# Kernel tuning notes

Measured on AMD Instinct MI355X. Metric: run time of the kernel, lower is better.

## Reference

```python
import jax, jax.numpy as jnp
import numpy as np

H = 16  # num_heads


def setup_inputs() -> dict:
    key = jax.random.key(0)
    ks = jax.random.split(key, 12)
    B, S, D = 2, 2048, 1024
    init = lambda k, shape: (jax.random.normal(k, shape, dtype=jnp.float32) * 0.02)
    return {
        "x": jax.random.normal(ks[0], (B, S, D), dtype=jnp.float32),
        "wq": init(ks[1], (D, D)), "bq": init(ks[2], (D,)),
        "wk": init(ks[3], (D, D)), "bk": init(ks[4], (D,)),
        "wv": init(ks[5], (D, D)), "bv": init(ks[6], (D,)),
        "wo": init(ks[7], (D, D)), "bo": init(ks[8], (D,)),
        "w3d": init(ks[9], (3, D)), "b3d": init(ks[10], (3,)),
    }


def _pairwise_l2(pos):
    # pos: [B,S,3] -> [B,S,S] Euclidean distance (safe sqrt: zero grad at 0, like torch.cdist)
    sq = jnp.sum((pos[:, :, None, :] - pos[:, None, :, :]) ** 2, axis=-1)
    safe = jnp.where(sq > 0, sq, 1.0)
    return jnp.where(sq > 0, jnp.sqrt(safe), 0.0)


def reference(x, wq, bq, wk, bk, wv, bv, wo, bo, w3d, b3d):
    B, S, D = x.shape
    hd = D // H
    scale = 1.0 / (hd ** 0.5)
    # V projection -> [B,H,S,hd]  (Q/K are computed in torch forward but unused in APPROX scores)
    V = (x @ wv.T + bv).reshape(B, S, H, hd).transpose(0, 2, 1, 3)
    # 3D semantic positions and non-dot-product scores (identical across heads)
    pos = x @ w3d.T + b3d                      # [B,S,3]
    dist = _pairwise_l2(pos)                   # [B,S,S]
    scores = -dist[:, None, :, :] * scale      # [B,H,S,S] (broadcast over heads)
    causal = jnp.triu(jnp.ones((S, S), dtype=bool), k=1)
    scores = jnp.where(causal[None, None], -jnp.inf, scores)
    attn = jax.nn.softmax(scores, axis=-1)
    attn = jnp.nan_to_num(attn, nan=0.0)
    out = jnp.einsum('bhqk,bhkd->bhqd', attn, V)  # [B,H,S,hd]
    out = out.transpose(0, 2, 1, 3).reshape(B, S, D)
    return out @ wo.T + bo
```

## Files before the change

### kernel.cpp

```cpp
#include <hip/hip_runtime.h>
#include <hip/hip_bf16.h>
#include <stdint.h>


typedef __attribute__((ext_vector_type(8))) short bf16x8;
typedef __attribute__((ext_vector_type(4))) float f32x4;
typedef __attribute__((ext_vector_type(4))) unsigned short us4;

#define AS1(p) (const __attribute__((address_space(1))) unsigned int*)(p)
#define AS3(p) (__attribute__((address_space(3))) unsigned int*)(p)

__device__ __forceinline__ unsigned short f2bf(float f) {
  union { float f; unsigned u; } v; v.f = f;
  unsigned r = v.u + 0x7FFFu + ((v.u >> 16) & 1u);
  return (unsigned short)(r >> 16);
}

__global__ void k_prep(const float* __restrict__ x, const float* __restrict__ wv,
                       const float* __restrict__ wo, const float* __restrict__ bv,
                       const float* __restrict__ bo, const float* __restrict__ w3d,
                       const float* __restrict__ b3d,
                       unsigned short* __restrict__ xT, unsigned short* __restrict__ wvT,
                       unsigned short* __restrict__ wob, float* __restrict__ cvec,
                       float* __restrict__ pos) {
  __shared__ __align__(16) float lsm[64 * 68];
  const int bx = blockIdx.x, t = threadIdx.x;
  if (bx < 1024) {
    const int b = bx >> 9, rest = bx & 511, st = rest >> 4, dt = rest & 15;
    const int s0 = st * 64, d0 = dt * 64;
    const int r = t >> 2, c4 = t & 3;
    const float* src = x + (size_t)(b * 2048 + s0 + r) * 1024 + d0;
    float (*ld)[68] = (float(*)[68])lsm;
    #pragma unroll
    for (int p = 0; p < 4; p++)
      *(float4*)&ld[r][(c4 + 4 * p) * 4] = ((const float4*)src)[c4 + 4 * p];
    __syncthreads();
    #pragma unroll
    for (int p = 0; p < 4; p++) {
      const int dl = (t >> 4) + (p << 4);
      us4 o;
      #pragma unroll
      for (int k = 0; k < 4; k++)
        ((unsigned short*)&o)[k] = f2bf(ld[(t & 15) * 4 + k][dl]);
      *(us4*)(xT + ((size_t)b << 21) + (size_t)(d0 + dl) * 2048 + s0 + (t & 15) * 4) = o;
    }
  } else if (bx < 2048) {
    const int bb = bx - 1024, tr = bb >> 5, tc = bb & 31;
    const int r = t >> 5, c = t & 31;
    float (*ld)[33] = (float(*)[33])lsm;
    #pragma unroll
    for (int rr = r; rr < 32; rr += 8)
      ld[rr][c] = wv[(size_t)(tr * 32 + rr) * 1024 + tc * 32 + c];
    __syncthreads();
    #pragma unroll
    for (int rr = r; rr < 32; rr += 8)
      wvT[(size_t)(tc * 32 + rr) * 1024 + tr * 32 + c] = f2bf(ld[c][rr]);
  } else if (bx < 3072) {
    const int oo = bx - 2048;
    const float4 w = ((const float4*)(wo + (size_t)oo * 1024))[t];
    us4 ob; ob.x = f2bf(w.x); ob.y = f2bf(w.y); ob.z = f2bf(w.z); ob.w = f2bf(w.w);
    ((us4*)(wob + (size_t)oo * 1024))[t] = ob;
    const float4 b = ((const float4*)bv)[t];
    float a = w.x * b.x + w.y * b.y + w.z * b.z + w.w * b.w;
    #pragma unroll
    for (int off = 32; off; off >>= 1) a += __shfl_down(a, off, 64);
    if ((t & 63) == 0) lsm[t >> 6] = a;
    __syncthreads();
    if (t == 0) cvec[oo] = lsm[0] + lsm[1] + lsm[2] + lsm[3] + bo[oo];
  } else {
    const int row = bx - 3072;
    const float4 xv = ((const float4*)(x + (size_t)row * 1024))[t];
    const float4 w0 = ((const float4*)(w3d))[t];
    const float4 w1 = ((const float4*)(w3d + 1024))[t];
    const float4 w2 = ((const float4*)(w3d + 2048))[t];
    float a0 = xv.x*w0.x + xv.y*w0.y + xv.z*w0.z + xv.w*w0.w;
    float a1 = xv.x*w1.x + xv.y*w1.y + xv.z*w1.z + xv.w*w1.w;
    float a2 = xv.x*w2.x + xv.y*w2.y + xv.z*w2.z + xv.w*w2.w;
    #pragma unroll
    for (int off = 32; off; off >>= 1) {
      a0 += __shfl_down(a0, off, 64);
      a1 += __shfl_down(a1, off, 64);
      a2 += __shfl_down(a2, off, 64);
    }
    if ((t & 63) == 0) { lsm[(t >> 6) * 3] = a0; lsm[(t >> 6) * 3 + 1] = a1; lsm[(t >> 6) * 3 + 2] = a2; }
    __syncthreads();
    if (t == 0) {
      pos[(size_t)row*3 + 0] = lsm[0] + lsm[3] + lsm[6] + lsm[9]  + b3d[0];
      pos[(size_t)row*3 + 1] = lsm[1] + lsm[4] + lsm[7] + lsm[10] + b3d[1];
      pos[(size_t)row*3 + 2] = lsm[2] + lsm[5] + lsm[8] + lsm[11] + b3d[2];
    }
  }
}

__global__ void k_attn(const float* __restrict__ pos, unsigned short* __restrict__ Ab) {
  const int row = blockIdx.x;
  const int q = row & 2047, bb = row >> 11;
  const float* pb = pos + ((size_t)bb << 11) * 3;
  const float qx = pb[q*3], qy = pb[q*3+1], qz = pb[q*3+2];
  const float4* pb4 = (const float4*)pb;
  const int jmax = ((q >> 7) + 1) << 7;
  float v[2][4];
  float sum = 0.f;
  #pragma unroll
  for (int cc = 0; cc < 2; cc++) {
    const int j0 = (cc << 10) + (threadIdx.x << 2);
    float e0 = 0.f, e1 = 0.f, e2 = 0.f, e3 = 0.f;
    if (j0 < jmax) {
      const float4 A4 = pb4[3*(j0 >> 2)], B4 = pb4[3*(j0 >> 2) + 1], C4 = pb4[3*(j0 >> 2) + 2];
      const float px[4] = {A4.x, A4.w, B4.z, C4.y};
      const float py[4] = {A4.y, B4.x, B4.w, C4.z};
      const float pz[4] = {A4.z, B4.y, C4.x, C4.w};
      float ee[4];
      #pragma unroll
      for (int u = 0; u < 4; u++) {
        float e = 0.f;
        if (j0 + u <= q) {
          float dx = qx - px[u], dy = qy - py[u], dz = qz - pz[u];
          float sq = fmaf(dx, dx, fmaf(dy, dy, dz*dz));
          float d = sq > 0.f ? sqrtf(sq) : 0.f;
          e = __expf(-0.125f * d);
        }
        ee[u] = e;
      }
      e0 = ee[0]; e1 = ee[1]; e2 = ee[2]; e3 = ee[3];
    }
    v[cc][0] = e0; v[cc][1] = e1; v[cc][2] = e2; v[cc][3] = e3;
    sum += e0 + e1 + e2 + e3;
  }
  #pragma unroll
  for (int off = 32; off; off >>= 1) sum += __shfl_down(sum, off, 64);
  __shared__ float red[4];
  if ((threadIdx.x & 63) == 0) red[threadIdx.x >> 6] = sum;
  __syncthreads();
  const float inv = 1.f / (red[0] + red[1] + red[2] + red[3]);
  unsigned short* orow = Ab + (size_t)row * 2048;
  #pragma unroll
  for (int cc = 0; cc < 2; cc++) {
    const int j0 = (cc << 10) + (threadIdx.x << 2);
    if (j0 < jmax) {
      us4 o;
      o.x = f2bf(v[cc][0]*inv); o.y = f2bf(v[cc][1]*inv);
      o.z = f2bf(v[cc][2]*inv); o.w = f2bf(v[cc][3]*inv);
      *(us4*)(orow + j0) = o;
    }
  }
}

template<int BM, int BN, int WM, int WN>
__device__ __forceinline__ void gemm_db(
    const unsigned short* __restrict__ A, int lda,
    const unsigned short* __restrict__ Bt, int ldb,
    int m0, int n0, int kmax,
    unsigned short* lds, f32x4* acc) {
  constexpr int WAVES = WM * WN;
  constexpr int FI = BM / (WM * 16), FJ = BN / (WN * 16);
  constexpr int CPW = ((BM + BN) / 8) / WAVES;
  constexpr int BUFSZ = (BM + BN) * 64;
  const int tid = threadIdx.x, l = tid & 63, w = tid >> 6;
  const int wm = w & (WM - 1), wn = w / WM;
  const int gcol = ((l & 7) ^ (l >> 3)) << 3;

  auto stage = [&](int buf, int k0) {
    unsigned short* base = lds + buf * BUFSZ;
    #pragma unroll
    for (int e = 0; e < CPW; ++e) {
      const int c = w * CPW + e;
      const unsigned short* src;
      unsigned short* dst;
      if (c < BM / 8) {
        src = A + (size_t)(m0 + c*8 + (l >> 3)) * lda + k0 + gcol;
        dst = base + c * 512;
      } else {
        const int cb = c - BM / 8;
        src = Bt + (size_t)(n0 + cb*8 + (l >> 3)) * ldb + k0 + gcol;
        dst = base + BM * 64 + cb * 512;
      }
      __builtin_amdgcn_global_load_lds(AS1(src), AS3(dst), 16, 0, 0);
    }
  };

  auto compute = [&](int buf) {
    unsigned short* lA = lds + buf * BUFSZ;
    unsigned short* lB = lA + BM * 64;
    #pragma unroll
    for (int h = 0; h < 2; ++h) {
      const int slot = ((h << 2) | (l >> 4)) ^ (l & 7);
      bf16x8 af[FI], bfr[FJ];
      #pragma unroll
      for (int i = 0; i < FI; ++i) {
        const int ar = wm * (BM / WM) + i * 16 + (l & 15);
        af[i] = *(const bf16x8*)&lA[ar * 64 + slot * 8];
      }
      #pragma unroll
      for (int j = 0; j < FJ; ++j) {
        const int br = wn * (BN / WN) + j * 16 + (l & 15);
        bfr[j] = *(const bf16x8*)&lB[br * 64 + slot * 8];
      }
      #pragma unroll
      for (int i = 0; i < FI; ++i)
        #pragma unroll
        for (int j = 0; j < FJ; ++j)
          acc[i * FJ + j] = __builtin_amdgcn_mfma_f32_16x16x32_bf16(af[i], bfr[j], acc[i * FJ + j], 0, 0, 0);
    }
  };

  const int NT = kmax >> 6;
  stage(0, 0);
  int cur = 0;
  for (int t = 0; t < NT; ++t) {
    if (t + 1 < NT) {
      stage(cur ^ 1, (t + 1) << 6);
      static_assert(CPW == 4 || CPW == 6 || CPW == 8, "vmcnt literal");
      if constexpr (CPW == 4) asm volatile("s_waitcnt vmcnt(4) lgkmcnt(0)" ::: "memory");
      else if constexpr (CPW == 6) asm volatile("s_waitcnt vmcnt(6) lgkmcnt(0)" ::: "memory");
      else asm volatile("s_waitcnt vmcnt(8) lgkmcnt(0)" ::: "memory");
    } else {
      asm volatile("s_waitcnt vmcnt(0) lgkmcnt(0)" ::: "memory");
    }
    __builtin_amdgcn_s_barrier();
    compute(cur);
    __builtin_amdgcn_s_barrier();
    cur ^= 1;
  }
}

__global__ __launch_bounds__(256, 3) void k_gemm_axwc(
    const unsigned short* __restrict__ Ab, const unsigned short* __restrict__ xT,
    unsigned short* __restrict__ Axb,
    const unsigned short* __restrict__ wob, const unsigned short* __restrict__ wvT,
    unsigned short* __restrict__ Wcs) {
  __shared__ __align__(16) unsigned short lds[2 * (128 + 64) * 64];
  const int bx = blockIdx.x;
  const int l = threadIdx.x & 63, w = threadIdx.x >> 6;
  const int wm = w & 1, wn = w >> 1;
  if (bx < 512) {
    f32x4 acc[8] = {};
    const int xcd = bx & 7, rest = bx >> 3;
    const int g = rest >> 4, n0i = rest & 15;
    const int mi = (g < 2) ? (15 - xcd) : xcd;
    const int b = g & 1;
    const int m0 = mi << 7, n0 = n0i << 6;
    const unsigned short* A  = Ab + ((size_t)b << 22);
    const unsigned short* Bt = xT + ((size_t)b << 21);
    gemm_db<128, 64, 2, 2>(A, 2048, Bt, 2048, m0, n0, (mi + 1) << 7, lds, acc);
    unsigned short* Obase = Axb + ((size_t)b << 11) * 1024;
    #pragma unroll
    for (int i = 0; i < 4; i++) {
      const int r0 = m0 + wm*64 + i*16 + ((l >> 4) << 2);
      #pragma unroll
      for (int j = 0; j < 2; j++) {
        const int cidx = n0 + wn*32 + j*16 + (l & 15);
        #pragma unroll
        for (int t = 0; t < 4; t++)
          Obase[(size_t)(r0 + t) * 1024 + cidx] = f2bf(acc[i*2 + j][t]);
      }
    }
  } else {
    f32x4 acc[4] = {};
    const int g = bx - 512;
    const int m0 = (g & 15) * 64, n0 = (g >> 4) * 64;
    gemm_db<64, 64, 2, 2>(wob, 1024, wvT, 1024, m0, n0, 1024, lds, acc);
    #pragma unroll
    for (int i = 0; i < 2; i++) {
      const int r0 = m0 + wm*32 + i*16 + ((l >> 4) << 2);
      #pragma unroll
      for (int j = 0; j < 2; j++) {
        const int cidx = n0 + wn*32 + j*16 + (l & 15);
        #pragma unroll
        for (int t = 0; t < 4; t++)
          Wcs[(size_t)(r0 + t) * 1024 + cidx] = f2bf(acc[i*2 + j][t]);
      }
    }
  }
}

__global__ __launch_bounds__(256, 2) void k_gemm_out(
    const unsigned short* __restrict__ Axb, const unsigned short* __restrict__ Wcs,
    const float* __restrict__ cvec, float* __restrict__ out) {
  __shared__ __align__(16) unsigned short lds[2 * (128 + 128) * 64];
  f32x4 acc[16] = {};
  const int m0 = blockIdx.x * 128, n0 = blockIdx.y * 128;
  gemm_db<128, 128, 2, 2>(Axb, 1024, Wcs, 1024, m0, n0, 1024, lds, acc);
  const int l = threadIdx.x & 63, w = threadIdx.x >> 6;
  const int wm = w & 1, wn = w >> 1;
  #pragma unroll
  for (int i = 0; i < 4; i++) {
    const int r0 = m0 + wm*64 + i*16 + ((l >> 4) << 2);
    #pragma unroll
    for (int j = 0; j < 4; j++) {
      const int cidx = n0 + wn*64 + j*16 + (l & 15);
      const float cv = cvec[cidx];
      #pragma unroll
      for (int t = 0; t < 4; t++)
        out[(size_t)(r0 + t) * 1024 + cidx] = acc[i*4 + j][t] + cv;
    }
  }
}

extern "C" void kernel_launch(void* const* d_in, const int* in_sizes, int n_in,
                              void* d_out, int out_size, void* d_ws, size_t ws_size,
                              hipStream_t stream) {
  const float* x   = (const float*)d_in[0];
  const float* wv  = (const float*)d_in[5];
  const float* bv  = (const float*)d_in[6];
  const float* wo  = (const float*)d_in[7];
  const float* bo  = (const float*)d_in[8];
  const float* w3d = (const float*)d_in[9];
  const float* b3d = (const float*)d_in[10];
  float* out = (float*)d_out;

  char* ws = (char*)d_ws;
  unsigned short* xT  = (unsigned short*)(ws);
  unsigned short* wvT = (unsigned short*)(ws + ( 8u << 20));
  unsigned short* wob = (unsigned short*)(ws + (10u << 20));
  unsigned short* Wcs = (unsigned short*)(ws + (12u << 20));
  unsigned short* Axb = (unsigned short*)(ws + (14u << 20));
  unsigned short* Ab  = (unsigned short*)(ws + (22u << 20));
  float*          pos = (float*)(ws + (38u << 20));
  float*          cvec= (float*)(ws + (39u << 20));

  k_prep<<<7168, 256, 0, stream>>>(x, wv, wo, bv, bo, w3d, b3d, xT, wvT, wob, cvec, pos);
  k_attn<<<4096, 256, 0, stream>>>(pos, Ab);
  k_gemm_axwc<<<768, 256, 0, stream>>>(Ab, xT, Axb, wob, wvT, Wcs);
  k_gemm_out<<<dim3(32, 8), 256, 0, stream>>>(Axb, Wcs, cvec, out);
}
```

Before: 57.67 us.

## Replace double-buffered GEMM loop with three-stage LDS ring in axwc kernel

Adds a gemm_ring variant that keeps two K-tiles of global-to-LDS loads in flight, using three LDS buffers, and issues each prefetch right after the barrier. This removes the second barrier per iteration. The goal is to hide more global load latency behind MFMA work. In exchange LDS per block grows by half and launch bounds drop from 3 to 2 blocks per CU, so occupancy may fall.

```diff
diff --git a/kernel.cpp b/kernel.cpp
--- a/kernel.cpp
+++ b/kernel.cpp
@@ -147,6 +147,85 @@
 }
 
 template<int BM, int BN, int WM, int WN>
+__device__ __forceinline__ void gemm_ring(
+    const unsigned short* __restrict__ A, int lda,
+    const unsigned short* __restrict__ Bt, int ldb,
+    int m0, int n0, int kmax,
+    unsigned short* lds, f32x4* acc) {
+  constexpr int WAVES = WM * WN;
+  constexpr int FI = BM / (WM * 16), FJ = BN / (WN * 16);
+  constexpr int CPW = ((BM + BN) / 8) / WAVES;
+  constexpr int BUFSZ = (BM + BN) * 64;
+  const int tid = threadIdx.x, l = tid & 63, w = tid >> 6;
+  const int wm = w & (WM - 1), wn = w / WM;
+  const int gcol = ((l & 7) ^ (l >> 3)) << 3;
+
+  auto stage = [&](int buf, int k0) {
+    unsigned short* base = lds + buf * BUFSZ;
+    #pragma unroll
+    for (int e = 0; e < CPW; ++e) {
+      const int c = w * CPW + e;
+      const unsigned short* src;
+      unsigned short* dst;
+      if (c < BM / 8) {
+        src = A + (size_t)(m0 + c*8 + (l >> 3)) * lda + k0 + gcol;
+        dst = base + c * 512;
+      } else {
+        const int cb = c - BM / 8;
+        src = Bt + (size_t)(n0 + cb*8 + (l >> 3)) * ldb + k0 + gcol;
+        dst = base + BM * 64 + cb * 512;
+      }
+      __builtin_amdgcn_global_load_lds(AS1(src), AS3(dst), 16, 0, 0);
+    }
+  };
+
+  auto compute = [&](int buf) {
+    unsigned short* lA = lds + buf * BUFSZ;
+    unsigned short* lB = lA + BM * 64;
+    #pragma unroll
+    for (int h = 0; h < 2; ++h) {
+      const int slot = ((h << 2) | (l >> 4)) ^ (l & 7);
+      bf16x8 af[FI], bfr[FJ];
+      #pragma unroll
+      for (int i = 0; i < FI; ++i) {
+        const int ar = wm * (BM / WM) + i * 16 + (l & 15);
+        af[i] = *(const bf16x8*)&lA[ar * 64 + slot * 8];
+      }
+      #pragma unroll
+      for (int j = 0; j < FJ; ++j) {
+        const int br = wn * (BN / WN) + j * 16 + (l & 15);
+        bfr[j] = *(const bf16x8*)&lB[br * 64 + slot * 8];
+      }
+      #pragma unroll
+      for (int i = 0; i < FI; ++i)
+        #pragma unroll
+        for (int j = 0; j < FJ; ++j)
+          acc[i * FJ + j] = __builtin_amdgcn_mfma_f32_16x16x32_bf16(af[i], bfr[j], acc[i * FJ + j], 0, 0, 0);
+    }
+  };
+
+  const int NT = kmax >> 6;
+  stage(0, 0);
+  if (NT > 1) stage(1, 64);
+  int cur = 0, nxt2 = 2;
+  for (int t = 0; t < NT; ++t) {
+    if (t < NT - 1) {
+      static_assert(CPW == 4 || CPW == 6 || CPW == 8, "vmcnt literal");
+      if constexpr (CPW == 4) asm volatile("s_waitcnt vmcnt(4) lgkmcnt(0)" ::: "memory");
+      else if constexpr (CPW == 6) asm volatile("s_waitcnt vmcnt(6) lgkmcnt(0)" ::: "memory");
+      else asm volatile("s_waitcnt vmcnt(8) lgkmcnt(0)" ::: "memory");
+    } else {
+      asm volatile("s_waitcnt vmcnt(0) lgkmcnt(0)" ::: "memory");
+    }
+    __builtin_amdgcn_s_barrier();
+    if (t + 2 < NT) stage(nxt2, (t + 2) << 6);
+    compute(cur);
+    cur = cur == 2 ? 0 : cur + 1;
+    nxt2 = nxt2 == 2 ? 0 : nxt2 + 1;
+  }
+}
+
+template<int BM, int BN, int WM, int WN>
 __device__ __forceinline__ void gemm_db(
     const unsigned short* __restrict__ A, int lda,
     const unsigned short* __restrict__ Bt, int ldb,
@@ -224,12 +303,12 @@
   }
 }
 
-__global__ __launch_bounds__(256, 3) void k_gemm_axwc(
+__global__ __launch_bounds__(256, 2) void k_gemm_axwc(
     const unsigned short* __restrict__ Ab, const unsigned short* __restrict__ xT,
     unsigned short* __restrict__ Axb,
     const unsigned short* __restrict__ wob, const unsigned short* __restrict__ wvT,
     unsigned short* __restrict__ Wcs) {
-  __shared__ __align__(16) unsigned short lds[2 * (128 + 64) * 64];
+  __shared__ __align__(16) unsigned short lds[3 * (128 + 64) * 64];
   const int bx = blockIdx.x;
   const int l = threadIdx.x & 63, w = threadIdx.x >> 6;
   const int wm = w & 1, wn = w >> 1;
@@ -242,7 +321,7 @@
     const int m0 = mi << 7, n0 = n0i << 6;
     const unsigned short* A  = Ab + ((size_t)b << 22);
     const unsigned short* Bt = xT + ((size_t)b << 21);
-    gemm_db<128, 64, 2, 2>(A, 2048, Bt, 2048, m0, n0, (mi + 1) << 7, lds, acc);
+    gemm_ring<128, 64, 2, 2>(A, 2048, Bt, 2048, m0, n0, (mi + 1) << 7, lds, acc);
     unsigned short* Obase = Axb + ((size_t)b << 11) * 1024;
     #pragma unroll
     for (int i = 0; i < 4; i++) {
@@ -259,7 +338,7 @@
     f32x4 acc[4] = {};
     const int g = bx - 512;
     const int m0 = (g & 15) * 64, n0 = (g >> 4) * 64;
-    gemm_db<64, 64, 2, 2>(wob, 1024, wvT, 1024, m0, n0, 1024, lds, acc);
+    gemm_ring<64, 64, 2, 2>(wob, 1024, wvT, 1024, m0, n0, 1024, lds, acc);
     #pragma unroll
     for (int i = 0; i < 2; i++) {
       const int r0 = m0 + wm*32 + i*16 + ((l >> 4) << 2);
```

Result: no change. 57.09 us (-1.0%).
